# Optimization experiments

Hardware: AMD Instinct MI355X
Metric: run time of the kernel (lower is better)

Reference implementation:

```python
import jax, jax.numpy as jnp
import numpy as np

J, P, L, C = 24, 8, 128, 8
N = 65536


def grid_sample(image, grid):
    # Bilinear grid_sample, align_corners=True, border-clamped indices
    # image: (B, C, H, W), grid: (B, Hg, Wg, 2) with (x=width, y=height) in [-1, 1]
    B, Cc, H, W = image.shape
    Hg, Wg = grid.shape[1], grid.shape[2]
    ix = (grid[..., 0] + 1.0) * 0.5 * (W - 1)
    iy = (grid[..., 1] + 1.0) * 0.5 * (H - 1)
    ix0 = jnp.floor(ix)
    iy0 = jnp.floor(iy)
    ix1 = ix0 + 1.0
    iy1 = iy0 + 1.0
    w_nw = (ix1 - ix) * (iy1 - iy)
    w_ne = (ix - ix0) * (iy1 - iy)
    w_sw = (ix1 - ix) * (iy - iy0)
    w_se = (ix - ix0) * (iy - iy0)
    ix0c = jnp.clip(ix0, 0, W - 1).astype(jnp.int32)
    ix1c = jnp.clip(ix1, 0, W - 1).astype(jnp.int32)
    iy0c = jnp.clip(iy0, 0, H - 1).astype(jnp.int32)
    iy1c = jnp.clip(iy1, 0, H - 1).astype(jnp.int32)
    img = image.reshape(B, Cc, H * W)

    def gather(iyc, ixc):
        idx = (iyc * W + ixc).reshape(B, 1, Hg * Wg)
        return jnp.take_along_axis(img, idx, axis=2)  # (B, Cc, Hg*Wg)

    out = (gather(iy0c, ix0c) * w_nw.reshape(B, 1, -1)
           + gather(iy0c, ix1c) * w_ne.reshape(B, 1, -1)
           + gather(iy1c, ix0c) * w_sw.reshape(B, 1, -1)
           + gather(iy1c, ix1c) * w_se.reshape(B, 1, -1))
    return out.reshape(B, Cc, Hg, Wg)


def sample(feat_lines, grid, pid):
    # feat_lines: (J, P, Lh, Lw, C); grid: (1, N, 1, 2)
    Jn, Pn, Lh, Lw, Cn = feat_lines.shape
    B, Np = grid.shape[:2]
    lines = jnp.transpose(feat_lines[:, pid], (0, 3, 1, 2)).reshape(1, Jn * Cn, Lh, Lw)
    feat = grid_sample(lines, grid)  # (1, J*C, N, 1)
    # raw reshape, replicating torch .view(B, N, J, C) on contiguous (1, J*C, N, 1)
    return feat.reshape(B, Np, Jn, Cn)


def setup_inputs():
    key = jax.random.key(0)
    ks = jax.random.split(key, 5)
    s = 0.01
    return {
        "feat_lines_x": jax.random.uniform(ks[0], (J, P, L, L, C), jnp.float32, -s, s),
        "feat_lines_y": jax.random.uniform(ks[1], (J, P, L, L, C), jnp.float32, -s, s),
        "feat_lines_z": jax.random.uniform(ks[2], (J, P, L, L, C), jnp.float32, -s, s),
        "query_points": jax.random.uniform(ks[3], (N, 3), jnp.float32),
        "scale": jnp.ones((3,), jnp.float32),
        "skinning_weight": jax.random.uniform(ks[4], (N, J), jnp.float32),
        "id": 3,
    }


def reference(feat_lines_x, feat_lines_y, feat_lines_z, query_points, scale, skinning_weight, id):
    qp = query_points - jnp.mean(query_points, axis=0)[None, :]  # (N, 3)
    x = qp[:, 0] / (scale[0] / 2)
    y = qp[:, 1] / (scale[1] / 2)
    z = qp[:, 2] / (scale[2] / 2)
    yx = jnp.stack((y, x), axis=1)[None, :, None, :]  # (1, N, 1, 2)
    xz = jnp.stack((x, z), axis=1)[None, :, None, :]
    zy = jnp.stack((z, y), axis=1)[None, :, None, :]
    feat_x = sample(feat_lines_x, yx, id)
    feat_y = sample(feat_lines_y, zy, id)
    feat_z = sample(feat_lines_z, xz, id)
    feat = jnp.concatenate([feat_x, feat_y, feat_z], axis=3)  # (1, N, J, 3C)
    return jnp.einsum('bnjc,nj->bnc', feat, skinning_weight)  # (1, N, 3C)
```

## Files before the change

### kernel.cpp

```cpp
#include <hip/hip_runtime.h>

constexpr int NPQ = 65536;
constexpr int JJ = 24, CC = 8, PP = 8, LL = 128;
constexpr int OUTC = 24;
constexpr int TOTAL = NPQ * OUTC;
constexpr int NCHP = 192;
constexpr size_t PLANE_H = 16384;
constexpr size_t FH_ELEMS = (size_t)576 * PLANE_H;

typedef _Float16 h2 __attribute__((ext_vector_type(2)));


__global__ __launch_bounds__(256) void k_partial(const float* __restrict__ qp,
                                                 float* __restrict__ partial) {
    __shared__ float s[3][256];
    int t = threadIdx.x;
    int n = blockIdx.x * 256 + t;
    s[0][t] = qp[n * 3 + 0];
    s[1][t] = qp[n * 3 + 1];
    s[2][t] = qp[n * 3 + 2];
    __syncthreads();
    for (int off = 128; off > 0; off >>= 1) {
        if (t < off) {
            s[0][t] += s[0][t + off];
            s[1][t] += s[1][t + off];
            s[2][t] += s[2][t + off];
        }
        __syncthreads();
    }
    if (t == 0) {
        partial[blockIdx.x * 4 + 0] = s[0][0];
        partial[blockIdx.x * 4 + 1] = s[1][0];
        partial[blockIdx.x * 4 + 2] = s[2][0];
    }
}

__global__ __launch_bounds__(256) void k_final(const float* __restrict__ partial,
                                               float* __restrict__ mean) {
    __shared__ float s[3][256];
    int t = threadIdx.x;
    s[0][t] = partial[t * 4 + 0];
    s[1][t] = partial[t * 4 + 1];
    s[2][t] = partial[t * 4 + 2];
    __syncthreads();
    for (int off = 128; off > 0; off >>= 1) {
        if (t < off) {
            s[0][t] += s[0][t + off];
            s[1][t] += s[1][t + off];
            s[2][t] += s[2][t + off];
        }
        __syncthreads();
    }
    if (t < 3) mean[t] = s[t][0] * (1.0f / 65536.0f);
}

__global__ __launch_bounds__(256) void k_prep_feat(
    const float* __restrict__ fx_, const float* __restrict__ fy_,
    const float* __restrict__ fz_, const int* __restrict__ idp,
    unsigned int* __restrict__ FhW) {
    int bid = blockIdx.x;
    int g = bid >> 5;
    int rg = bid & 31;
    int p = g / 24, jimg = g - p * 24;
    const float* feat = (p == 0) ? fx_ : (p == 1) ? fy_ : fz_;
    int pid = *idp;
    int t = threadIdx.x;
    int ly = t >> 6, k = t & 63;
    int y = rg * 4 + ly;
    int x2 = k * 2;
    const float* src = feat + (((size_t)jimg * PP + (size_t)pid) * 16384 +
                               (size_t)(y * 128 + x2)) * 8;
    float4 a0 = *(const float4*)src;
    float4 a1 = *(const float4*)(src + 4);
    float4 b0 = *(const float4*)(src + 8);
    float4 b1 = *(const float4*)(src + 12);
    float av[8] = {a0.x, a0.y, a0.z, a0.w, a1.x, a1.y, a1.z, a1.w};
    float bv[8] = {b0.x, b0.y, b0.z, b0.w, b1.x, b1.y, b1.z, b1.w};
#pragma unroll
    for (int c = 0; c < 8; ++c) {
        h2 w;
        w[0] = (_Float16)av[c];
        w[1] = (_Float16)bv[c];
        FhW[((size_t)g * 8 + c) * 8192 + (size_t)(y * 64 + k)] =
            __builtin_bit_cast(unsigned int, w);
    }
}

__global__ __launch_bounds__(256) void k_prep_coord(
    const float* __restrict__ qp, const float* __restrict__ scale,
    const float* __restrict__ mean, uint2* __restrict__ co) {
    int n = blockIdx.x * 256 + threadIdx.x;
    float qv[3] = {qp[n * 3 + 0], qp[n * 3 + 1], qp[n * 3 + 2]};
#pragma unroll
    for (int p = 0; p < 3; ++p) {
        int wc = (p + 1) - ((p + 1) >= 3 ? 3 : 0);
        int hc = p;
        float gw = (qv[wc] - mean[wc]) * (2.0f / scale[wc]);
        float gh = (qv[hc] - mean[hc]) * (2.0f / scale[hc]);
        float ixf = (gw + 1.0f) * 63.5f;
        float iyf = (gh + 1.0f) * 63.5f;
        float fx0 = floorf(ixf), fy0 = floorf(iyf);
        float fx = ixf - fx0, fy = iyf - fy0;
        int x0i = (int)fx0, y0i = (int)fy0;
        int xr, yr;
        float fxc, fyc;
        if (x0i < 0)        { xr = 0;   fxc = 0.0f; }
        else if (x0i > 126) { xr = 126; fxc = 1.0f; }
        else                { xr = x0i; fxc = fx;   }
        if (y0i < 0)        { yr = 0;   fyc = 0.0f; }
        else if (y0i > 126) { yr = 126; fyc = 1.0f; }
        else                { yr = y0i; fyc = fy;   }
        h2 f; f[0] = (_Float16)fxc; f[1] = (_Float16)fyc;
        uint2 e;
        e.x = (unsigned)(yr * 128 + xr);
        e.y = __builtin_bit_cast(unsigned int, f);
        co[((size_t)p << 16) + (size_t)n] = e;
    }
}

__device__ __forceinline__ float sample1(const unsigned int* sp, uint2 d) {
    unsigned lo_w = sp[d.x];
    unsigned hi_w = sp[d.x + 128];
    h2 f = __builtin_bit_cast(h2, d.y);
    h2 lo = __builtin_bit_cast(h2, lo_w);
    h2 hi = __builtin_bit_cast(h2, hi_w);
    _Float16 fy = f[1];
    h2 fy2; fy2[0] = fy; fy2[1] = fy;
    h2 oy2; oy2[0] = (_Float16)1.0f - fy; oy2[1] = oy2[0];
    h2 r = lo * oy2 + hi * fy2;
    float r0 = (float)r[0], r1 = (float)r[1];
    float fxf = (float)f[0];
    return fmaf(fxf, r1 - r0, r0);
}

__global__ __launch_bounds__(512) void k_fused(
    const unsigned int* __restrict__ FhW, const uint2* __restrict__ co,
    const float* __restrict__ sw, float* __restrict__ out,
    float* __restrict__ preb, float* __restrict__ postb) {
    int b = blockIdx.x;
    int Lid = (b & 7) * 144 + (b >> 3);
    int half = Lid & 1;
    int jcp = Lid >> 1;
    int p = jcp / NCHP;
    int jc = jcp - p * NCHP;

    __shared__ unsigned long long splane64[8192];
    {
        const unsigned int* src = FhW + (size_t)jcp * 8192;
        int tid = threadIdx.x;
#pragma unroll
        for (int q = 0; q < 16; ++q) {
            int idx = q * 512 + tid;
            int y = idx >> 6;
            int k = idx & 63;
            unsigned w = src[idx];
            unsigned wn = __shfl_down(w, 1, 64);
            unsigned hi16 = w >> 16;
            unsigned next16 = (k == 63) ? hi16 : (wn & 0xffffu);
            unsigned combined = hi16 | (next16 << 16);
            splane64[(size_t)(y * 64 + k)] =
                (unsigned long long)w | ((unsigned long long)combined << 32);
        }
    }
    __syncthreads();
    const unsigned int* sp = (const unsigned int*)splane64;

    int i0 = jc << 16;
    int r  = (jc % 3) * 64;
    int r1 = ((jc + 1) % 3) * 64;
    int npF_lo = (i0 + 191) / 192;
    int npF_hi = ((jc + 1) << 16) / 192;
    int cnt = npF_hi - npF_lo;
    int mid = npF_lo + (cnt >> 1);
    int loR = half ? mid : npF_lo;
    int hiR = half ? npF_hi : mid;
    bool hasPre  = (half == 0) && (r != 0);
    bool hasPost = (half == 1) && (r1 != 0);

    int nFull = (hiR - loR) * 8;
    int nTot = nFull + (hasPre ? 8 : 0) + (hasPost ? 8 : 0);
    const uint2* cop = co + ((size_t)p << 16);

    for (int k = threadIdx.x; k < nTot; k += 512) {
        if (k < nFull) {
            int np = loR + (k >> 3);
            int c = k & 7;
            const uint2* cb = cop + (np * 192 + c - i0);
            const float4* swv = (const float4*)(sw + (size_t)np * 24);
            float4 s0 = swv[0], s1 = swv[1], s2 = swv[2];
            float4 s3 = swv[3], s4 = swv[4], s5 = swv[5];
            float swreg[24] = {s0.x, s0.y, s0.z, s0.w, s1.x, s1.y, s1.z, s1.w,
                               s2.x, s2.y, s2.z, s2.w, s3.x, s3.y, s3.z, s3.w,
                               s4.x, s4.y, s4.z, s4.w, s5.x, s5.y, s5.z, s5.w};
            float acc = 0.0f;
#pragma unroll
            for (int j = 0; j < 24; ++j) {
                uint2 d = cb[j * 8];
                acc += swreg[j] * sample1(sp, d);
            }
            out[(size_t)np * 24 + p * 8 + c] = acc;
        } else {
            bool isPre = hasPre && (k < nFull + 8);
            int c = (k - nFull) & 7;
            int np = isPre ? (i0 / 192) : npF_hi;
            int jlo = isPre ? (r >> 3) : 0;
            int jhi = isPre ? 24 : (r1 >> 3);
            int n0 = np * 192 + c - i0;
            float acc = 0.0f;
            for (int j = jlo; j < jhi; ++j) {
                uint2 d = cop[n0 + j * 8];
                acc += sw[(size_t)np * 24 + j] * sample1(sp, d);
            }
            float* dst = isPre ? preb : postb;
            dst[(size_t)jcp * 8 + c] = acc;
        }
    }
}

__global__ __launch_bounds__(256) void k_fix(const float* __restrict__ preb,
                                             const float* __restrict__ postb,
                                             float* __restrict__ out) {
    int t = blockIdx.x * 256 + threadIdx.x;
    if (t >= 3 * 191 * 8) return;
    int c = t & 7;
    int rest = t >> 3;
    int jc = rest % 191;
    int p = rest / 191;
    if (((jc + 1) % 3) == 0) return;
    int np = ((jc + 1) << 16) / 192;
    out[(size_t)np * 24 + p * 8 + c] =
        postb[((size_t)p * NCHP + jc) * 8 + c] +
        preb[((size_t)p * NCHP + jc + 1) * 8 + c];
}

__global__ __launch_bounds__(256) void k_main(
    const float* __restrict__ featx, const float* __restrict__ featy,
    const float* __restrict__ featz, const float* __restrict__ qp,
    const float* __restrict__ scale, const float* __restrict__ sw,
    const int* __restrict__ idp, const float* __restrict__ mean,
    float* __restrict__ out) {
    int t = blockIdx.x * 256 + threadIdx.x;
    if (t >= TOTAL) return;
    int np = t / OUTC;
    int cp = t - np * OUTC;
    int p  = cp >> 3;
    int c  = cp & 7;
    const float* feat = (p == 0) ? featx : (p == 1) ? featy : featz;
    int pid = *idp;
    int wc = (p + 1) - ((p + 1) >= 3 ? 3 : 0);
    int hc = p;
    float mw = mean[wc], mh = mean[hc];
    float invw = 2.0f / scale[wc];
    float invh = 2.0f / scale[hc];
    const float* featpid = feat + (size_t)pid * (LL * LL * CC);
    int ibase = np * 192 + c;
    float acc = 0.0f;
#pragma unroll 4
    for (int j = 0; j < JJ; ++j) {
        int i  = ibase + j * 8;
        int jc = i >> 16;
        int n  = i & 65535;
        int jimg = jc >> 3;
        int cimg = jc & 7;
        const float* img = featpid + (size_t)jimg * (PP * LL * LL * CC) + cimg;
        float gw = (qp[n * 3 + wc] - mw) * invw;
        float gh = (qp[n * 3 + hc] - mh) * invh;
        float ixf = (gw + 1.0f) * 63.5f;
        float iyf = (gh + 1.0f) * 63.5f;
        float ix0 = floorf(ixf), iy0 = floorf(iyf);
        float fx = ixf - ix0, fy = iyf - iy0;
        int x0i = (int)ix0, y0i = (int)iy0;
        int x0 = min(127, max(0, x0i));
        int x1 = min(127, max(0, x0i + 1));
        int y0 = min(127, max(0, y0i));
        int y1 = min(127, max(0, y0i + 1));
        int r0 = y0 * (LL * CC);
        int r1 = y1 * (LL * CC);
        float v00 = img[r0 + x0 * CC];
        float v01 = img[r0 + x1 * CC];
        float v10 = img[r1 + x0 * CC];
        float v11 = img[r1 + x1 * CC];
        float omfx = 1.0f - fx, omfy = 1.0f - fy;
        float S = omfx * omfy * v00 + fx * omfy * v01 +
                  omfx * fy * v10 + fx * fy * v11;
        acc += sw[np * JJ + j] * S;
    }
    out[t] = acc;
}

extern "C" void kernel_launch(void* const* d_in, const int* in_sizes, int n_in,
                              void* d_out, int out_size, void* d_ws, size_t ws_size,
                              hipStream_t stream) {
    const float* featx = (const float*)d_in[0];
    const float* featy = (const float*)d_in[1];
    const float* featz = (const float*)d_in[2];
    const float* qp    = (const float*)d_in[3];
    const float* scale = (const float*)d_in[4];
    const float* sw    = (const float*)d_in[5];
    const int*   idp   = (const int*)d_in[6];
    float* out = (float*)d_out;

    size_t off_Fh = 0;
    size_t off_co = off_Fh + FH_ELEMS * 2;
    size_t off_pre = off_co + (size_t)3 * 65536 * 8;
    size_t off_post = off_pre + 576 * 8 * 4;
    size_t off_partial = off_post + 576 * 8 * 4;
    size_t off_mean = off_partial + 4096;
    size_t needed = off_mean + 16;

    if (ws_size >= needed) {
        char* wsb = (char*)d_ws;
        unsigned int* FhW = (unsigned int*)(wsb + off_Fh);
        uint2* co        = (uint2*)(wsb + off_co);
        float* preb      = (float*)(wsb + off_pre);
        float* postb     = (float*)(wsb + off_post);
        float* partial   = (float*)(wsb + off_partial);
        float* mean      = (float*)(wsb + off_mean);

        k_partial<<<256, 256, 0, stream>>>(qp, partial);
        k_final<<<1, 256, 0, stream>>>(partial, mean);
        k_prep_feat<<<2304, 256, 0, stream>>>(featx, featy, featz, idp, FhW);
        k_prep_coord<<<256, 256, 0, stream>>>(qp, scale, mean, co);
        k_fused<<<1152, 512, 0, stream>>>(FhW, co, sw, out, preb, postb);
        k_fix<<<18, 256, 0, stream>>>(preb, postb, out);
    } else {
        float* ws = (float*)d_ws;
        float* mean    = ws;
        float* partial = ws + 4;
        k_partial<<<256, 256, 0, stream>>>(qp, partial);
        k_final<<<1, 256, 0, stream>>>(partial, mean);
        k_main<<<(TOTAL + 255) / 256, 256, 0, stream>>>(
            featx, featy, featz, qp, scale, sw, idp, mean, out);
    }
}
```

Before: 64.86 us.

## Merge prep kernels, fp16 skinning weights, replace fix-up kernel with atomics

New measurement: 56.46 us. 1.15x faster.

```diff
diff --git a/kernel.cpp b/kernel.cpp
--- a/kernel.cpp
+++ b/kernel.cpp
@@ -10,34 +10,92 @@
 
 typedef _Float16 h2 __attribute__((ext_vector_type(2)));
 
-
-__global__ __launch_bounds__(256) void k_partial(const float* __restrict__ qp,
-                                                 float* __restrict__ partial) {
+__global__ __launch_bounds__(256) void k_prep_all(
+    const float* __restrict__ fx_, const float* __restrict__ fy_,
+    const float* __restrict__ fz_, const int* __restrict__ idp,
+    const float* __restrict__ qp, const float* __restrict__ sw,
+    unsigned int* __restrict__ FhW, unsigned short* __restrict__ swh,
+    float* __restrict__ partial) {
+    int bid = blockIdx.x;
+    int t = threadIdx.x;
+    if (bid < 2304) {
+        int g = bid >> 5;
+        int rg = bid & 31;
+        int p = g / 24, jimg = g - p * 24;
+        const float* feat = (p == 0) ? fx_ : (p == 1) ? fy_ : fz_;
+        int pid = *idp;
+        int ly = t >> 6, k = t & 63;
+        int y = rg * 4 + ly;
+        int x2 = k * 2;
+        const float* src = feat + (((size_t)jimg * PP + (size_t)pid) * 16384 +
+                                   (size_t)(y * 128 + x2)) * 8;
+        float4 a0 = *(const float4*)src;
+        float4 a1 = *(const float4*)(src + 4);
+        float4 b0 = *(const float4*)(src + 8);
+        float4 b1 = *(const float4*)(src + 12);
+        float av[8] = {a0.x, a0.y, a0.z, a0.w, a1.x, a1.y, a1.z, a1.w};
+        float bv[8] = {b0.x, b0.y, b0.z, b0.w, b1.x, b1.y, b1.z, b1.w};
+#pragma unroll
+        for (int c = 0; c < 8; ++c) {
+            h2 w;
+            w[0] = (_Float16)av[c];
+            w[1] = (_Float16)bv[c];
+            FhW[((size_t)g * 8 + c) * 8192 + (size_t)(y * 64 + k)] =
+                __builtin_bit_cast(unsigned int, w);
+        }
+    } else if (bid < 2560) {
+        __shared__ float s[3][256];
+        int n = (bid - 2304) * 256 + t;
+        s[0][t] = qp[n * 3 + 0];
+        s[1][t] = qp[n * 3 + 1];
+        s[2][t] = qp[n * 3 + 2];
+        __syncthreads();
+        for (int off = 128; off > 0; off >>= 1) {
+            if (t < off) {
+                s[0][t] += s[0][t + off];
+                s[1][t] += s[1][t + off];
+                s[2][t] += s[2][t + off];
+            }
+            __syncthreads();
+        }
+        if (t == 0) {
+            partial[(bid - 2304) * 4 + 0] = s[0][0];
+            partial[(bid - 2304) * 4 + 1] = s[1][0];
+            partial[(bid - 2304) * 4 + 2] = s[2][0];
+        }
+    } else {
+        int n = (bid - 2560) * 256 + t;
+        const float* s = sw + (size_t)n * 24;
+        float4 v0 = *(const float4*)(s);
+        float4 v1 = *(const float4*)(s + 4);
+        float4 v2 = *(const float4*)(s + 8);
+        float4 v3 = *(const float4*)(s + 12);
+        float4 v4 = *(const float4*)(s + 16);
+        float4 v5 = *(const float4*)(s + 20);
+        float vv[24] = {v0.x, v0.y, v0.z, v0.w, v1.x, v1.y, v1.z, v1.w,
+                        v2.x, v2.y, v2.z, v2.w, v3.x, v3.y, v3.z, v3.w,
+                        v4.x, v4.y, v4.z, v4.w, v5.x, v5.y, v5.z, v5.w};
+        unsigned u[12];
+#pragma unroll
+        for (int q = 0; q < 12; ++q) {
+            h2 w;
+            w[0] = (_Float16)vv[q * 2];
+            w[1] = (_Float16)vv[q * 2 + 1];
+            u[q] = __builtin_bit_cast(unsigned, w);
+        }
+        uint4* dst = (uint4*)(swh + (size_t)n * 24);
+        dst[0] = make_uint4(u[0], u[1], u[2], u[3]);
+        dst[1] = make_uint4(u[4], u[5], u[6], u[7]);
+        dst[2] = make_uint4(u[8], u[9], u[10], u[11]);
+    }
+}
+
+__global__ __launch_bounds__(256) void k_coord(
+    const float* __restrict__ qp, const float* __restrict__ scale,
+    const float* __restrict__ partial, uint2* __restrict__ co,
+    float* __restrict__ out) {
     __shared__ float s[3][256];
-    int t = threadIdx.x;
-    int n = blockIdx.x * 256 + t;
-    s[0][t] = qp[n * 3 + 0];
-    s[1][t] = qp[n * 3 + 1];
-    s[2][t] = qp[n * 3 + 2];
-    __syncthreads();
-    for (int off = 128; off > 0; off >>= 1) {
-        if (t < off) {
-            s[0][t] += s[0][t + off];
-            s[1][t] += s[1][t + off];
-            s[2][t] += s[2][t + off];
-        }
-        __syncthreads();
-    }
-    if (t == 0) {
-        partial[blockIdx.x * 4 + 0] = s[0][0];
-        partial[blockIdx.x * 4 + 1] = s[1][0];
-        partial[blockIdx.x * 4 + 2] = s[2][0];
-    }
-}
-
-__global__ __launch_bounds__(256) void k_final(const float* __restrict__ partial,
-                                               float* __restrict__ mean) {
-    __shared__ float s[3][256];
+    __shared__ float smean[3];
     int t = threadIdx.x;
     s[0][t] = partial[t * 4 + 0];
     s[1][t] = partial[t * 4 + 1];
@@ -51,52 +109,29 @@
         }
         __syncthreads();
     }
-    if (t < 3) mean[t] = s[t][0] * (1.0f / 65536.0f);
-}
-
-__global__ __launch_bounds__(256) void k_prep_feat(
-    const float* __restrict__ fx_, const float* __restrict__ fy_,
-    const float* __restrict__ fz_, const int* __restrict__ idp,
-    unsigned int* __restrict__ FhW) {
-    int bid = blockIdx.x;
-    int g = bid >> 5;
-    int rg = bid & 31;
-    int p = g / 24, jimg = g - p * 24;
-    const float* feat = (p == 0) ? fx_ : (p == 1) ? fy_ : fz_;
-    int pid = *idp;
-    int t = threadIdx.x;
-    int ly = t >> 6, k = t & 63;
-    int y = rg * 4 + ly;
-    int x2 = k * 2;
-    const float* src = feat + (((size_t)jimg * PP + (size_t)pid) * 16384 +
-                               (size_t)(y * 128 + x2)) * 8;
-    float4 a0 = *(const float4*)src;
-    float4 a1 = *(const float4*)(src + 4);
-    float4 b0 = *(const float4*)(src + 8);
-    float4 b1 = *(const float4*)(src + 12);
-    float av[8] = {a0.x, a0.y, a0.z, a0.w, a1.x, a1.y, a1.z, a1.w};
-    float bv[8] = {b0.x, b0.y, b0.z, b0.w, b1.x, b1.y, b1.z, b1.w};
-#pragma unroll
-    for (int c = 0; c < 8; ++c) {
-        h2 w;
-        w[0] = (_Float16)av[c];
-        w[1] = (_Float16)bv[c];
-        FhW[((size_t)g * 8 + c) * 8192 + (size_t)(y * 64 + k)] =
-            __builtin_bit_cast(unsigned int, w);
-    }
-}
-
-__global__ __launch_bounds__(256) void k_prep_coord(
-    const float* __restrict__ qp, const float* __restrict__ scale,
-    const float* __restrict__ mean, uint2* __restrict__ co) {
-    int n = blockIdx.x * 256 + threadIdx.x;
+    if (t < 3) smean[t] = s[t][0] * (1.0f / 65536.0f);
+    __syncthreads();
+
+    int gt = blockIdx.x * 256 + t;
+    if (gt < 3 * 191 * 8) {
+        int c = gt & 7;
+        int rest = gt >> 3;
+        int jcb = rest % 191;
+        int p = rest / 191;
+        if (((jcb + 1) % 3) != 0) {
+            int np = ((jcb + 1) << 16) / 192;
+            out[(size_t)np * 24 + p * 8 + c] = 0.0f;
+        }
+    }
+
+    int n = blockIdx.x * 256 + t;
     float qv[3] = {qp[n * 3 + 0], qp[n * 3 + 1], qp[n * 3 + 2]};
 #pragma unroll
     for (int p = 0; p < 3; ++p) {
         int wc = (p + 1) - ((p + 1) >= 3 ? 3 : 0);
         int hc = p;
-        float gw = (qv[wc] - mean[wc]) * (2.0f / scale[wc]);
-        float gh = (qv[hc] - mean[hc]) * (2.0f / scale[hc]);
+        float gw = (qv[wc] - smean[wc]) * (2.0f / scale[wc]);
+        float gh = (qv[hc] - smean[hc]) * (2.0f / scale[hc]);
         float ixf = (gw + 1.0f) * 63.5f;
         float iyf = (gh + 1.0f) * 63.5f;
         float fx0 = floorf(ixf), fy0 = floorf(iyf);
@@ -133,10 +168,15 @@
     return fmaf(fxf, r1 - r0, r0);
 }
 
+__device__ __forceinline__ void up2(float* d, unsigned u) {
+    h2 v = __builtin_bit_cast(h2, u);
+    d[0] = (float)v[0];
+    d[1] = (float)v[1];
+}
+
 __global__ __launch_bounds__(512) void k_fused(
     const unsigned int* __restrict__ FhW, const uint2* __restrict__ co,
-    const float* __restrict__ sw, float* __restrict__ out,
-    float* __restrict__ preb, float* __restrict__ postb) {
+    const unsigned short* __restrict__ swh, float* __restrict__ out) {
     int b = blockIdx.x;
     int Lid = (b & 7) * 144 + (b >> 3);
     int half = Lid & 1;
@@ -186,12 +226,15 @@
             int np = loR + (k >> 3);
             int c = k & 7;
             const uint2* cb = cop + (np * 192 + c - i0);
-            const float4* swv = (const float4*)(sw + (size_t)np * 24);
-            float4 s0 = swv[0], s1 = swv[1], s2 = swv[2];
-            float4 s3 = swv[3], s4 = swv[4], s5 = swv[5];
-            float swreg[24] = {s0.x, s0.y, s0.z, s0.w, s1.x, s1.y, s1.z, s1.w,
-                               s2.x, s2.y, s2.z, s2.w, s3.x, s3.y, s3.z, s3.w,
-                               s4.x, s4.y, s4.z, s4.w, s5.x, s5.y, s5.z, s5.w};
+            const uint4* sw4 = (const uint4*)(swh + (size_t)np * 24);
+            uint4 wA = sw4[0], wB = sw4[1], wC = sw4[2];
+            float swreg[24];
+            up2(swreg + 0,  wA.x); up2(swreg + 2,  wA.y);
+            up2(swreg + 4,  wA.z); up2(swreg + 6,  wA.w);
+            up2(swreg + 8,  wB.x); up2(swreg + 10, wB.y);
+            up2(swreg + 12, wB.z); up2(swreg + 14, wB.w);
+            up2(swreg + 16, wC.x); up2(swreg + 18, wC.y);
+            up2(swreg + 20, wC.z); up2(swreg + 22, wC.w);
             float acc = 0.0f;
 #pragma unroll
             for (int j = 0; j < 24; ++j) {
@@ -209,28 +252,56 @@
             float acc = 0.0f;
             for (int j = jlo; j < jhi; ++j) {
                 uint2 d = cop[n0 + j * 8];
-                acc += sw[(size_t)np * 24 + j] * sample1(sp, d);
+                float wj =
+                    (float)__builtin_bit_cast(_Float16, swh[(size_t)np * 24 + j]);
+                acc += wj * sample1(sp, d);
             }
-            float* dst = isPre ? preb : postb;
-            dst[(size_t)jcp * 8 + c] = acc;
-        }
-    }
-}
-
-__global__ __launch_bounds__(256) void k_fix(const float* __restrict__ preb,
-                                             const float* __restrict__ postb,
-                                             float* __restrict__ out) {
-    int t = blockIdx.x * 256 + threadIdx.x;
-    if (t >= 3 * 191 * 8) return;
-    int c = t & 7;
-    int rest = t >> 3;
-    int jc = rest % 191;
-    int p = rest / 191;
-    if (((jc + 1) % 3) == 0) return;
-    int np = ((jc + 1) << 16) / 192;
-    out[(size_t)np * 24 + p * 8 + c] =
-        postb[((size_t)p * NCHP + jc) * 8 + c] +
-        preb[((size_t)p * NCHP + jc + 1) * 8 + c];
+            atomicAdd(&out[(size_t)np * 24 + p * 8 + c], acc);
+        }
+    }
+}
+
+__global__ __launch_bounds__(256) void k_partial(const float* __restrict__ qp,
+                                                 float* __restrict__ partial) {
+    __shared__ float s[3][256];
+    int t = threadIdx.x;
+    int n = blockIdx.x * 256 + t;
+    s[0][t] = qp[n * 3 + 0];
+    s[1][t] = qp[n * 3 + 1];
+    s[2][t] = qp[n * 3 + 2];
+    __syncthreads();
+    for (int off = 128; off > 0; off >>= 1) {
+        if (t < off) {
+            s[0][t] += s[0][t + off];
+            s[1][t] += s[1][t + off];
+            s[2][t] += s[2][t + off];
+        }
+        __syncthreads();
+    }
+    if (t == 0) {
+        partial[blockIdx.x * 4 + 0] = s[0][0];
+        partial[blockIdx.x * 4 + 1] = s[1][0];
+        partial[blockIdx.x * 4 + 2] = s[2][0];
+    }
+}
+
+__global__ __launch_bounds__(256) void k_finalm(const float* __restrict__ partial,
+                                                float* __restrict__ mean) {
+    __shared__ float s[3][256];
+    int t = threadIdx.x;
+    s[0][t] = partial[t * 4 + 0];
+    s[1][t] = partial[t * 4 + 1];
+    s[2][t] = partial[t * 4 + 2];
+    __syncthreads();
+    for (int off = 128; off > 0; off >>= 1) {
+        if (t < off) {
+            s[0][t] += s[0][t + off];
+            s[1][t] += s[1][t + off];
+            s[2][t] += s[2][t + off];
+        }
+        __syncthreads();
+    }
+    if (t < 3) mean[t] = s[t][0] * (1.0f / 65536.0f);
 }
 
 __global__ __launch_bounds__(256) void k_main(
@@ -302,33 +373,28 @@
 
     size_t off_Fh = 0;
     size_t off_co = off_Fh + FH_ELEMS * 2;
-    size_t off_pre = off_co + (size_t)3 * 65536 * 8;
-    size_t off_post = off_pre + 576 * 8 * 4;
-    size_t off_partial = off_post + 576 * 8 * 4;
+    size_t off_sw = off_co + (size_t)3 * 65536 * 8;
+    size_t off_partial = off_sw + (size_t)65536 * 24 * 2;
     size_t off_mean = off_partial + 4096;
     size_t needed = off_mean + 16;
 
     if (ws_size >= needed) {
         char* wsb = (char*)d_ws;
-        unsigned int* FhW = (unsigned int*)(wsb + off_Fh);
-        uint2* co        = (uint2*)(wsb + off_co);
-        float* preb      = (float*)(wsb + off_pre);
-        float* postb     = (float*)(wsb + off_post);
-        float* partial   = (float*)(wsb + off_partial);
-        float* mean      = (float*)(wsb + off_mean);
-
-        k_partial<<<256, 256, 0, stream>>>(qp, partial);
-        k_final<<<1, 256, 0, stream>>>(partial, mean);
-        k_prep_feat<<<2304, 256, 0, stream>>>(featx, featy, featz, idp, FhW);
-        k_prep_coord<<<256, 256, 0, stream>>>(qp, scale, mean, co);
-        k_fused<<<1152, 512, 0, stream>>>(FhW, co, sw, out, preb, postb);
-        k_fix<<<18, 256, 0, stream>>>(preb, postb, out);
+        unsigned int* FhW   = (unsigned int*)(wsb + off_Fh);
+        uint2* co           = (uint2*)(wsb + off_co);
+        unsigned short* swh = (unsigned short*)(wsb + off_sw);
+        float* partial      = (float*)(wsb + off_partial);
+
+        k_prep_all<<<2816, 256, 0, stream>>>(featx, featy, featz, idp, qp, sw,
+                                             FhW, swh, partial);
+        k_coord<<<256, 256, 0, stream>>>(qp, scale, partial, co, out);
+        k_fused<<<1152, 512, 0, stream>>>(FhW, co, swh, out);
     } else {
         float* ws = (float*)d_ws;
         float* mean    = ws;
         float* partial = ws + 4;
         k_partial<<<256, 256, 0, stream>>>(qp, partial);
-        k_final<<<1, 256, 0, stream>>>(partial, mean);
+        k_finalm<<<1, 256, 0, stream>>>(partial, mean);
         k_main<<<(TOTAL + 255) / 256, 256, 0, stream>>>(
             featx, featy, featz, qp, scale, sw, idp, mean, out);
     }
```
